# Kernel optimization log

Hardware: AMD Instinct MI355X
Metric: run time of the kernel (lower is better)

## Reference

```python
import jax, jax.numpy as jnp
import numpy as np

N = 20000        # nodes
E = 640000       # edges (before self-loops)
F_IN = 128
HID = 64
HEADS = 4
F_OUT = 128
G = 64           # graphs in batch
NEG_SLOPE = 0.2  # PyG GATConv leaky_relu default


def setup_inputs() -> dict:
    key = jax.random.key(0)
    ks = jax.random.split(key, 16)
    s = 0.05
    x = jax.random.normal(ks[0], (N, F_IN), jnp.float32)
    edge_index = jax.random.randint(ks[1], (2, E), 0, N, dtype=jnp.int64)
    batch = jnp.sort(jax.random.randint(ks[2], (N,), 0, G, dtype=jnp.int64))
    # layer 1: F_IN -> HID x HEADS (concat)
    W1 = jax.random.normal(ks[3], (F_IN, HEADS * HID), jnp.float32) * s
    a_src1 = jax.random.normal(ks[4], (HEADS, HID), jnp.float32) * s
    a_dst1 = jax.random.normal(ks[5], (HEADS, HID), jnp.float32) * s
    b1 = jnp.zeros((HEADS * HID,), jnp.float32)
    # layer 2: HEADS*HID -> HID x HEADS (concat)
    W2 = jax.random.normal(ks[6], (HEADS * HID, HEADS * HID), jnp.float32) * s
    a_src2 = jax.random.normal(ks[7], (HEADS, HID), jnp.float32) * s
    a_dst2 = jax.random.normal(ks[8], (HEADS, HID), jnp.float32) * s
    b2 = jnp.zeros((HEADS * HID,), jnp.float32)
    # layer 3: HEADS*HID -> F_OUT, heads=1, concat=False (mean)
    W3 = jax.random.normal(ks[9], (HEADS * HID, F_OUT), jnp.float32) * s
    a_src3 = jax.random.normal(ks[10], (1, F_OUT), jnp.float32) * s
    a_dst3 = jax.random.normal(ks[11], (1, F_OUT), jnp.float32) * s
    b3 = jnp.zeros((F_OUT,), jnp.float32)
    return dict(x=x, edge_index=edge_index, batch=batch,
                W1=W1, a_src1=a_src1, a_dst1=a_dst1, b1=b1,
                W2=W2, a_src2=a_src2, a_dst2=a_dst2, b2=b2,
                W3=W3, a_src3=a_src3, a_dst3=a_dst3, b3=b3)


def _gat_layer(x, src, dst, W, a_s, a_d, b, heads, concat):
    n = x.shape[0]
    h = (x @ W).reshape(n, heads, -1)                # [N,H,C]
    alpha_s = (h * a_s[None]).sum(-1)                # [N,H]
    alpha_d = (h * a_d[None]).sum(-1)                # [N,H]
    e = jax.nn.leaky_relu(alpha_s[src] + alpha_d[dst], NEG_SLOPE)  # [E,H]
    # segment softmax over incoming edges of each dst node
    m = jax.ops.segment_max(e, dst, num_segments=n)
    ex = jnp.exp(e - m[dst])
    denom = jax.ops.segment_sum(ex, dst, num_segments=n)
    alpha = ex / (denom[dst] + 1e-16)                # [E,H]
    out = jax.ops.segment_sum(alpha[:, :, None] * h[src], dst, num_segments=n)  # [N,H,C]
    out = out.reshape(n, -1) if concat else out.mean(axis=1)
    return out + b


def reference(x, edge_index, batch, W1, a_src1, a_dst1, b1,
              W2, a_src2, a_dst2, b2, W3, a_src3, a_dst3, b3):
    n = x.shape[0]
    # add self loops (PyG GATConv default add_self_loops=True)
    loop = jnp.arange(n, dtype=edge_index.dtype)
    src = jnp.concatenate([edge_index[0], loop])
    dst = jnp.concatenate([edge_index[1], loop])

    h = _gat_layer(x, src, dst, W1, a_src1, a_dst1, b1, HEADS, True)
    h = jax.nn.elu(h)
    h = _gat_layer(h, src, dst, W2, a_src2, a_dst2, b2, HEADS, True)
    h = jax.nn.elu(h)
    h = _gat_layer(h, src, dst, W3, a_src3, a_dst3, b3, 1, False)

    # global mean pool over graphs
    sums = jax.ops.segment_sum(h, batch, num_segments=G)
    cnts = jax.ops.segment_sum(jnp.ones((n, 1), h.dtype), batch, num_segments=G)
    graph_embedding = sums / jnp.maximum(cnts, 1.0)
    return graph_embedding, h
```

## Files before the change

### kernel.cpp

```cpp
#include <hip/hip_runtime.h>
#include <hip/hip_bf16.h>
#include <math.h>

#define N_NODES 20000
#define N_EDGES 640000
#define ET_EDGES (N_EDGES + N_NODES)
#define G_GRAPHS 64
#define NEG_SLOPE 0.2f


__global__ void hist_dst(const int* __restrict__ ei, int* __restrict__ cnt,
                         const int* __restrict__ batch, int* __restrict__ gstart) {
    int j = blockIdx.x * blockDim.x + threadIdx.x;
    if (blockIdx.x == 0 && threadIdx.x <= G_GRAPHS) {
        int g = threadIdx.x;
        int lo = 0, hi = N_NODES;
        while (lo < hi) {
            int mid = (lo + hi) >> 1;
            if (batch[mid] < g) lo = mid + 1; else hi = mid;
        }
        gstart[g] = lo;
    }
    if (j >= ET_EDGES) return;
    int d = (j < N_EDGES) ? ei[N_EDGES + j] : (j - N_EDGES);
    atomicAdd(&cnt[d], 1);
}

__global__ __launch_bounds__(1024) void scan_rowptr(const int* __restrict__ cnt,
                                                    int* __restrict__ row_ptr) {
    __shared__ int sums[1024];
    const int n = N_NODES;
    const int CH = (n + 1023) / 1024;
    int t = threadIdx.x;
    int base = t * CH;
    int s = 0;
    for (int i = 0; i < CH; ++i) {
        int idx = base + i;
        if (idx < n) s += cnt[idx];
    }
    sums[t] = s;
    __syncthreads();
    for (int o = 1; o < 1024; o <<= 1) {
        int v = (t >= o) ? sums[t - o] : 0;
        __syncthreads();
        sums[t] += v;
        __syncthreads();
    }
    int run = (t == 0) ? 0 : sums[t - 1];
    for (int i = 0; i < CH; ++i) {
        int idx = base + i;
        if (idx < n) { row_ptr[idx] = run; run += cnt[idx]; }
    }
    if (t == 1023) row_ptr[n] = sums[1023];
}

__global__ void fill_csr(const int* __restrict__ ei, const int* __restrict__ row_ptr,
                         int* __restrict__ cur, int* __restrict__ col) {
    int j = blockIdx.x * blockDim.x + threadIdx.x;
    if (j >= ET_EDGES) return;
    int s, d;
    if (j < N_EDGES) { s = ei[j]; d = ei[N_EDGES + j]; }
    else             { s = d = j - N_EDGES; }
    int pos = row_ptr[d] + atomicAdd(&cur[d], 1);
    col[pos] = s;
}


__global__ __launch_bounds__(256) void sgemm64(const float* __restrict__ A,
                                               const float* __restrict__ B,
                                               float* __restrict__ C,
                                               int M, int K, int Nc) {
    __shared__ float As[16][64];
    __shared__ float Bs[16][64];
    int bm = blockIdx.x * 64;
    int bn = blockIdx.y * 64;
    int t = threadIdx.x;
    int tr = t >> 2, tq = t & 3;
    int bkr = t >> 4, bnq = t & 15;
    int tm = (t >> 4) * 4;
    int tn = (t & 15) * 4;
    float acc[4][4] = {};
    for (int k0 = 0; k0 < K; k0 += 16) {
        int ar = bm + tr;
        float4 av = make_float4(0.f, 0.f, 0.f, 0.f);
        if (ar < M) av = *(const float4*)&A[(size_t)ar * K + k0 + tq * 4];
        As[tq * 4 + 0][tr] = av.x;
        As[tq * 4 + 1][tr] = av.y;
        As[tq * 4 + 2][tr] = av.z;
        As[tq * 4 + 3][tr] = av.w;
        float4 bv = *(const float4*)&B[(size_t)(k0 + bkr) * Nc + bn + bnq * 4];
        *(float4*)&Bs[bkr][bnq * 4] = bv;
        __syncthreads();
        #pragma unroll
        for (int k = 0; k < 16; ++k) {
            float a[4], b[4];
            *(float4*)a = *(const float4*)&As[k][tm];
            *(float4*)b = *(const float4*)&Bs[k][tn];
            #pragma unroll
            for (int i = 0; i < 4; ++i)
                #pragma unroll
                for (int j = 0; j < 4; ++j)
                    acc[i][j] = fmaf(a[i], b[j], acc[i][j]);
        }
        __syncthreads();
    }
    #pragma unroll
    for (int i = 0; i < 4; ++i) {
        int r = bm + tm + i;
        if (r < M) {
            float4 o = make_float4(acc[i][0], acc[i][1], acc[i][2], acc[i][3]);
            *(float4*)&C[(size_t)r * Nc + bn + tn] = o;
        }
    }
}


template <int HEADS, int C>
__global__ __launch_bounds__(256) void node_alpha2(const float* __restrict__ h,
                                                   const float* __restrict__ a_src,
                                                   const float* __restrict__ a_dst,
                                                   float* __restrict__ asT,
                                                   float* __restrict__ adT) {
    constexpr int F = HEADS * C;
    constexpr int VEC = F / 64;
    constexpr int LPH = C / VEC;
    int wid = threadIdx.x >> 6, lane = threadIdx.x & 63;
    int v = blockIdx.x * 4 + wid;
    if (v >= N_NODES) return;
    const float* hp = h + (size_t)v * F + lane * VEC;
    float ps = 0.f, pd = 0.f;
    #pragma unroll
    for (int c = 0; c < VEC; ++c) {
        float hv = hp[c];
        ps = fmaf(hv, a_src[lane * VEC + c], ps);
        pd = fmaf(hv, a_dst[lane * VEC + c], pd);
    }
    #pragma unroll
    for (int o = LPH / 2; o; o >>= 1) {
        ps += __shfl_xor(ps, o);
        pd += __shfl_xor(pd, o);
    }
    if ((lane & (LPH - 1)) == 0) {
        int head = lane / LPH;
        asT[head * N_NODES + v] = ps;
        adT[head * N_NODES + v] = pd;
    }
}


template <int NSLICE, int SCH, int F, int HEADS, bool DO_ELU>
__global__ __launch_bounds__(256) void gat_aggregate_sliced(
        const float* __restrict__ h,
        const float* __restrict__ asT,
        const float* __restrict__ adT,
        const int* __restrict__ row_ptr,
        const int* __restrict__ col,
        const float* __restrict__ bias,
        float* __restrict__ out) {
    constexpr int CL = SCH / 4;
    constexpr int E  = 64 / CL;
    constexpr int CPH = F / HEADS;
    __shared__ int   s_off[4][64];
    __shared__ float s_p[4][64];
    int slice = blockIdx.x & (NSLICE - 1);
    int ng = blockIdx.x >> 2;
    int wid = threadIdx.x >> 6, lane = threadIdx.x & 63;
    int v = ng * 4 + wid;
    if (v >= N_NODES) return;
    int head = (slice * SCH) / CPH;
    int eg = lane / CL, cl = lane % CL;
    int r0 = row_ptr[v], r1 = row_ptr[v + 1];
    float ad = adT[head * N_NODES + v];
    const float* asrc = asT + head * N_NODES;
    float acc[4] = {};
    float lsum = 0.f;
    const char* hb = (const char*)(h + slice * SCH + cl * 4);

#define GATHER4(gg)                                                        \
    {                                                                      \
        int k0 = ((gg) + 0) * E + eg;                                      \
        int k1 = ((gg) + 1) * E + eg;                                      \
        int k2 = ((gg) + 2) * E + eg;                                      \
        int k3 = ((gg) + 3) * E + eg;                                      \
        float p0 = s_p[wid][k0]; int o0 = s_off[wid][k0];                  \
        float p1 = s_p[wid][k1]; int o1 = s_off[wid][k1];                  \
        float p2 = s_p[wid][k2]; int o2 = s_off[wid][k2];                  \
        float p3 = s_p[wid][k3]; int o3 = s_off[wid][k3];                  \
        float4 h0 = *(const float4*)(hb + o0);                             \
        float4 h1 = *(const float4*)(hb + o1);                             \
        float4 h2 = *(const float4*)(hb + o2);                             \
        float4 h3 = *(const float4*)(hb + o3);                             \
        acc[0] = fmaf(p0, h0.x, acc[0]);                                   \
        acc[1] = fmaf(p0, h0.y, acc[1]);                                   \
        acc[2] = fmaf(p0, h0.z, acc[2]);                                   \
        acc[3] = fmaf(p0, h0.w, acc[3]);                                   \
        acc[0] = fmaf(p1, h1.x, acc[0]);                                   \
        acc[1] = fmaf(p1, h1.y, acc[1]);                                   \
        acc[2] = fmaf(p1, h1.z, acc[2]);                                   \
        acc[3] = fmaf(p1, h1.w, acc[3]);                                   \
        acc[0] = fmaf(p2, h2.x, acc[0]);                                   \
        acc[1] = fmaf(p2, h2.y, acc[1]);                                   \
        acc[2] = fmaf(p2, h2.z, acc[2]);                                   \
        acc[3] = fmaf(p2, h2.w, acc[3]);                                   \
        acc[0] = fmaf(p3, h3.x, acc[0]);                                   \
        acc[1] = fmaf(p3, h3.y, acc[1]);                                   \
        acc[2] = fmaf(p3, h3.z, acc[2]);                                   \
        acc[3] = fmaf(p3, h3.w, acc[3]);                                   \
    }

    for (int base = r0; base < r1; base += 64) {
        int j = base + lane;
        bool valid = j < r1;
        int s = col[valid ? j : r0];
        float e = asrc[s] + ad;
        e = (e > 0.f) ? e : NEG_SLOPE * e;
        float p = valid ? __expf(e) : 0.f;
        lsum += p;
        s_p[wid][lane] = p;
        s_off[wid][lane] = s * (F * 4);

        int nk = min(64, r1 - base);
        int nkg = (nk + E - 1) / E;
        int g = 0;
        for (; g + 4 <= nkg; g += 4) GATHER4(g);
        if (g < nkg) GATHER4(g);
    }
#undef GATHER4

    #pragma unroll
    for (int o = 32; o; o >>= 1) lsum += __shfl_xor(lsum, o);
    #pragma unroll
    for (int c = 0; c < 4; ++c) {
        #pragma unroll
        for (int o = CL; o < 64; o <<= 1) acc[c] += __shfl_xor(acc[c], o);
    }
    if (eg == 0) {
        float inv = 1.f / (lsum + 1e-16f);
        #pragma unroll
        for (int c = 0; c < 4; ++c) {
            int ch = slice * SCH + cl * 4 + c;
            float o = acc[c] * inv + bias[ch];
            if (DO_ELU) o = (o > 0.f) ? o : expm1f(o);
            out[(size_t)v * F + ch] = o;
        }
    }
}


__global__ void pool_mean4(const float* __restrict__ hout, const int* __restrict__ gstart,
                           float* __restrict__ gout) {
    int g = blockIdx.x;
    int q = blockIdx.y;
    int c = threadIdx.x;
    int off = gstart[g], end = gstart[g + 1];
    float inv = 1.f / fmaxf((float)(end - off), 1.0f);
    float s = 0.f;
    for (int i = off + q; i < end; i += 4) s += hout[(size_t)i * 128 + c];
    atomicAdd(&gout[g * 128 + c], s * inv);
}


static inline size_t align_up(size_t x, size_t a) { return (x + a - 1) & ~(a - 1); }

extern "C" void kernel_launch(void* const* d_in, const int* in_sizes, int n_in,
                              void* d_out, int out_size, void* d_ws, size_t ws_size,
                              hipStream_t stream) {
    const float* x   = (const float*)d_in[0];
    const int*   ei  = (const int*)d_in[1];
    const int*   bat = (const int*)d_in[2];
    const float* W1  = (const float*)d_in[3];
    const float* as1 = (const float*)d_in[4];
    const float* ad1 = (const float*)d_in[5];
    const float* b1  = (const float*)d_in[6];
    const float* W2  = (const float*)d_in[7];
    const float* as2 = (const float*)d_in[8];
    const float* ad2 = (const float*)d_in[9];
    const float* b2  = (const float*)d_in[10];
    const float* W3  = (const float*)d_in[11];
    const float* as3 = (const float*)d_in[12];
    const float* ad3 = (const float*)d_in[13];
    const float* b3  = (const float*)d_in[14];

    float* gout = (float*)d_out;
    float* hout = (float*)d_out + G_GRAPHS * 128;

    char* w = (char*)d_ws;
    size_t o = 0;
    float* bufA = (float*)(w + o); o = align_up(o + (size_t)N_NODES * 256 * 4, 256);
    float* bufB = (float*)(w + o); o = align_up(o + (size_t)N_NODES * 256 * 4, 256);
    float* asv  = (float*)(w + o); o = align_up(o + (size_t)N_NODES * 4 * 4, 256);
    float* adv  = (float*)(w + o); o = align_up(o + (size_t)N_NODES * 4 * 4, 256);
    int* row_ptr = (int*)(w + o);  o = align_up(o + (size_t)(N_NODES + 1) * 4, 256);
    int* col     = (int*)(w + o);  o = align_up(o + (size_t)ET_EDGES * 4, 256);
    int* cnt     = (int*)(w + o);  o += (size_t)N_NODES * 4;
    int* cur     = (int*)(w + o);  o = align_up(o + (size_t)N_NODES * 4, 256);
    int* gstart  = (int*)(w + o);  o = align_up(o + (size_t)(G_GRAPHS + 1) * 4, 256);

    hipMemsetAsync(cnt, 0, (size_t)N_NODES * 8, stream);
    hipMemsetAsync(gout, 0, (size_t)G_GRAPHS * 128 * 4, stream);
    hist_dst<<<(ET_EDGES + 255) / 256, 256, 0, stream>>>(ei, cnt, bat, gstart);
    scan_rowptr<<<1, 1024, 0, stream>>>(cnt, row_ptr);
    fill_csr<<<(ET_EDGES + 255) / 256, 256, 0, stream>>>(ei, row_ptr, cur, col);

    dim3 g4(313, 4), g2(313, 2);
    int nb = (N_NODES + 3) / 4;
    int nbs = nb * 4;

    sgemm64<<<g4, 256, 0, stream>>>(x, W1, bufA, N_NODES, 128, 256);
    node_alpha2<4, 64><<<nb, 256, 0, stream>>>(bufA, as1, ad1, asv, adv);
    gat_aggregate_sliced<4, 64, 256, 4, true><<<nbs, 256, 0, stream>>>(
        bufA, asv, adv, row_ptr, col, b1, bufB);

    sgemm64<<<g4, 256, 0, stream>>>(bufB, W2, bufA, N_NODES, 256, 256);
    node_alpha2<4, 64><<<nb, 256, 0, stream>>>(bufA, as2, ad2, asv, adv);
    gat_aggregate_sliced<4, 64, 256, 4, true><<<nbs, 256, 0, stream>>>(
        bufA, asv, adv, row_ptr, col, b2, bufB);

    sgemm64<<<g2, 256, 0, stream>>>(bufB, W3, bufA, N_NODES, 256, 128);
    node_alpha2<1, 128><<<nb, 256, 0, stream>>>(bufA, as3, ad3, asv, adv);
    gat_aggregate_sliced<4, 32, 128, 1, false><<<nbs, 256, 0, stream>>>(
        bufA, asv, adv, row_ptr, col, b3, hout);

    pool_mean4<<<dim3(G_GRAPHS, 4), 128, 0, stream>>>(hout, gstart, gout);
}
```

Baseline: 459.3 us.

## Replace fp32 SIMT GEMMs with split-bf16 MFMA GEMMs fed by aggregate epilogue

Swaps the scalar FMA sgemm for a matrix-core GEMM that represents each fp32 operand as a hi+lo bf16 pair and accumulates three bf16 MFMA products to keep near-fp32 accuracy. The aggregation epilogue of layers 1 and 2 now writes the activations directly as hi/lo bf16 arrays, and x and the weights are split (weights also transposed) in small pre-pass kernels. This targets the FP32 ALU cost of the three dense projections. In exchange it adds extra launches and split passes, and accuracy drops slightly from the dropped lo*lo term.

Measured after the change: 433.2 us. 1.06x faster.

```diff
diff --git a/kernel.cpp b/kernel.cpp
--- a/kernel.cpp
+++ b/kernel.cpp
@@ -7,6 +7,19 @@
 #define ET_EDGES (N_EDGES + N_NODES)
 #define G_GRAPHS 64
 #define NEG_SLOPE 0.2f
+
+typedef __attribute__((ext_vector_type(8))) short s8v;
+typedef __attribute__((ext_vector_type(4))) float f4v;
+
+__device__ __forceinline__ unsigned short bf_hi(float f) {
+    union { float f; unsigned int u; } c; c.f = f;
+    unsigned int r = (c.u + 0x7fffu + ((c.u >> 16) & 1u)) >> 16;
+    return (unsigned short)r;
+}
+__device__ __forceinline__ float bf_f(unsigned short h) {
+    union { unsigned int u; float f; } c; c.u = ((unsigned int)h) << 16;
+    return c.f;
+}
 
 
 __global__ void hist_dst(const int* __restrict__ ei, int* __restrict__ cnt,
@@ -66,52 +79,110 @@
 }
 
 
-__global__ __launch_bounds__(256) void sgemm64(const float* __restrict__ A,
-                                               const float* __restrict__ B,
-                                               float* __restrict__ C,
-                                               int M, int K, int Nc) {
-    __shared__ float As[16][64];
-    __shared__ float Bs[16][64];
-    int bm = blockIdx.x * 64;
-    int bn = blockIdx.y * 64;
-    int t = threadIdx.x;
-    int tr = t >> 2, tq = t & 3;
-    int bkr = t >> 4, bnq = t & 15;
-    int tm = (t >> 4) * 4;
-    int tn = (t & 15) * 4;
-    float acc[4][4] = {};
-    for (int k0 = 0; k0 < K; k0 += 16) {
-        int ar = bm + tr;
-        float4 av = make_float4(0.f, 0.f, 0.f, 0.f);
-        if (ar < M) av = *(const float4*)&A[(size_t)ar * K + k0 + tq * 4];
-        As[tq * 4 + 0][tr] = av.x;
-        As[tq * 4 + 1][tr] = av.y;
-        As[tq * 4 + 2][tr] = av.z;
-        As[tq * 4 + 3][tr] = av.w;
-        float4 bv = *(const float4*)&B[(size_t)(k0 + bkr) * Nc + bn + bnq * 4];
-        *(float4*)&Bs[bkr][bnq * 4] = bv;
+__global__ void split_f32(const float* __restrict__ in, unsigned short* __restrict__ hi,
+                          unsigned short* __restrict__ lo, int n) {
+    int i = (blockIdx.x * blockDim.x + threadIdx.x) * 4;
+    if (i >= n) return;
+    float4 v = *(const float4*)&in[i];
+    ushort4 h, l;
+    h.x = bf_hi(v.x); l.x = bf_hi(v.x - bf_f(h.x));
+    h.y = bf_hi(v.y); l.y = bf_hi(v.y - bf_f(h.y));
+    h.z = bf_hi(v.z); l.z = bf_hi(v.z - bf_f(h.z));
+    h.w = bf_hi(v.w); l.w = bf_hi(v.w - bf_f(h.w));
+    *(ushort4*)&hi[i] = h;
+    *(ushort4*)&lo[i] = l;
+}
+
+__global__ void wsplit(const float* __restrict__ W, unsigned short* __restrict__ th,
+                       unsigned short* __restrict__ tl, int K, int Nc) {
+    int idx = blockIdx.x * blockDim.x + threadIdx.x;
+    if (idx >= K * Nc) return;
+    int k = idx / Nc, n = idx % Nc;
+    float v = W[idx];
+    unsigned short h = bf_hi(v);
+    th[n * K + k] = h;
+    tl[n * K + k] = bf_hi(v - bf_f(h));
+}
+
+
+#define LDT 40
+
+__global__ __launch_bounds__(256) void gemm_split(
+        const unsigned short* __restrict__ Ah, const unsigned short* __restrict__ Al,
+        const unsigned short* __restrict__ Bh, const unsigned short* __restrict__ Bl,
+        float* __restrict__ C, int M, int Nc, int K) {
+    __shared__ unsigned short lAh[128 * LDT];
+    __shared__ unsigned short lAl[128 * LDT];
+    __shared__ unsigned short lBh[64 * LDT];
+    __shared__ unsigned short lBl[64 * LDT];
+    int bm = blockIdx.x * 128, bn = blockIdx.y * 64;
+    int t = threadIdx.x, w = t >> 6, lane = t & 63;
+    int wm = (w >> 1) * 64, wn = (w & 1) * 32;
+
+    f4v acc[4][2] = {};
+
+    int sr = t >> 1, sk = (t & 1) << 4;
+    int br = t >> 2, bk = (t & 3) << 3;
+    int ar = bm + sr; if (ar >= M) ar = M - 1;
+    const unsigned short* pAh = Ah + (size_t)ar * K + sk;
+    const unsigned short* pAl = Al + (size_t)ar * K + sk;
+    const unsigned short* pBh = Bh + (size_t)(bn + br) * K + bk;
+    const unsigned short* pBl = Bl + (size_t)(bn + br) * K + bk;
+
+    int fr = lane & 15, fk = (lane >> 4) << 3;
+
+    for (int k0 = 0; k0 < K; k0 += 32) {
+        uint4 vh0 = *(const uint4*)(pAh + k0);
+        uint4 vh1 = *(const uint4*)(pAh + k0 + 8);
+        uint4 vl0 = *(const uint4*)(pAl + k0);
+        uint4 vl1 = *(const uint4*)(pAl + k0 + 8);
+        uint4 wh  = *(const uint4*)(pBh + k0);
+        uint4 wl  = *(const uint4*)(pBl + k0);
         __syncthreads();
-        #pragma unroll
-        for (int k = 0; k < 16; ++k) {
-            float a[4], b[4];
-            *(float4*)a = *(const float4*)&As[k][tm];
-            *(float4*)b = *(const float4*)&Bs[k][tn];
+        *(uint4*)&lAh[sr * LDT + sk]     = vh0;
+        *(uint4*)&lAh[sr * LDT + sk + 8] = vh1;
+        *(uint4*)&lAl[sr * LDT + sk]     = vl0;
+        *(uint4*)&lAl[sr * LDT + sk + 8] = vl1;
+        *(uint4*)&lBh[br * LDT + bk] = wh;
+        *(uint4*)&lBl[br * LDT + bk] = wl;
+        __syncthreads();
+
+        s8v a_h[4], a_l[4], b_h[2], b_l[2];
+        #pragma unroll
+        for (int mi = 0; mi < 4; ++mi) {
+            a_h[mi] = *(const s8v*)&lAh[(wm + mi * 16 + fr) * LDT + fk];
+            a_l[mi] = *(const s8v*)&lAl[(wm + mi * 16 + fr) * LDT + fk];
+        }
+        #pragma unroll
+        for (int nj = 0; nj < 2; ++nj) {
+            b_h[nj] = *(const s8v*)&lBh[(wn + nj * 16 + fr) * LDT + fk];
+            b_l[nj] = *(const s8v*)&lBl[(wn + nj * 16 + fr) * LDT + fk];
+        }
+        #pragma unroll
+        for (int mi = 0; mi < 4; ++mi)
             #pragma unroll
-            for (int i = 0; i < 4; ++i)
-                #pragma unroll
-                for (int j = 0; j < 4; ++j)
-                    acc[i][j] = fmaf(a[i], b[j], acc[i][j]);
-        }
-        __syncthreads();
-    }
+            for (int nj = 0; nj < 2; ++nj) {
+                acc[mi][nj] = __builtin_amdgcn_mfma_f32_16x16x32_bf16(
+                    a_h[mi], b_h[nj], acc[mi][nj], 0, 0, 0);
+                acc[mi][nj] = __builtin_amdgcn_mfma_f32_16x16x32_bf16(
+                    a_h[mi], b_l[nj], acc[mi][nj], 0, 0, 0);
+                acc[mi][nj] = __builtin_amdgcn_mfma_f32_16x16x32_bf16(
+                    a_l[mi], b_h[nj], acc[mi][nj], 0, 0, 0);
+            }
+    }
+
     #pragma unroll
-    for (int i = 0; i < 4; ++i) {
-        int r = bm + tm + i;
-        if (r < M) {
-            float4 o = make_float4(acc[i][0], acc[i][1], acc[i][2], acc[i][3]);
-            *(float4*)&C[(size_t)r * Nc + bn + tn] = o;
-        }
-    }
+    for (int mi = 0; mi < 4; ++mi)
+        #pragma unroll
+        for (int nj = 0; nj < 2; ++nj) {
+            int row0 = bm + wm + mi * 16 + (lane >> 4) * 4;
+            int colc = bn + wn + nj * 16 + (lane & 15);
+            #pragma unroll
+            for (int q = 0; q < 4; ++q) {
+                int r = row0 + q;
+                if (r < M) C[(size_t)r * Nc + colc] = acc[mi][nj][q];
+            }
+        }
 }
 
 
@@ -148,7 +219,7 @@
 }
 
 
-template <int NSLICE, int SCH, int F, int HEADS, bool DO_ELU>
+template <int NSLICE, int SCH, int F, int HEADS, bool DO_ELU, bool SPLIT>
 __global__ __launch_bounds__(256) void gat_aggregate_sliced(
         const float* __restrict__ h,
         const float* __restrict__ asT,
@@ -156,7 +227,9 @@
         const int* __restrict__ row_ptr,
         const int* __restrict__ col,
         const float* __restrict__ bias,
-        float* __restrict__ out) {
+        float* __restrict__ out,
+        unsigned short* __restrict__ oh,
+        unsigned short* __restrict__ ol) {
     constexpr int CL = SCH / 4;
     constexpr int E  = 64 / CL;
     constexpr int CPH = F / HEADS;
@@ -236,12 +309,25 @@
     }
     if (eg == 0) {
         float inv = 1.f / (lsum + 1e-16f);
+        int ch0 = slice * SCH + cl * 4;
+        float o4[4];
         #pragma unroll
         for (int c = 0; c < 4; ++c) {
-            int ch = slice * SCH + cl * 4 + c;
-            float o = acc[c] * inv + bias[ch];
+            float o = acc[c] * inv + bias[ch0 + c];
             if (DO_ELU) o = (o > 0.f) ? o : expm1f(o);
-            out[(size_t)v * F + ch] = o;
+            o4[c] = o;
+        }
+        if (SPLIT) {
+            ushort4 hv, lv;
+            hv.x = bf_hi(o4[0]); lv.x = bf_hi(o4[0] - bf_f(hv.x));
+            hv.y = bf_hi(o4[1]); lv.y = bf_hi(o4[1] - bf_f(hv.y));
+            hv.z = bf_hi(o4[2]); lv.z = bf_hi(o4[2] - bf_f(hv.z));
+            hv.w = bf_hi(o4[3]); lv.w = bf_hi(o4[3] - bf_f(hv.w));
+            *(ushort4*)&oh[(size_t)v * F + ch0] = hv;
+            *(ushort4*)&ol[(size_t)v * F + ch0] = lv;
+        } else {
+            *(float4*)&out[(size_t)v * F + ch0] =
+                make_float4(o4[0], o4[1], o4[2], o4[3]);
         }
     }
 }
@@ -286,8 +372,17 @@
 
     char* w = (char*)d_ws;
     size_t o = 0;
-    float* bufA = (float*)(w + o); o = align_up(o + (size_t)N_NODES * 256 * 4, 256);
-    float* bufB = (float*)(w + o); o = align_up(o + (size_t)N_NODES * 256 * 4, 256);
+    float* bufA = (float*)(w + o);           o = align_up(o + (size_t)N_NODES * 256 * 4, 256);
+    unsigned short* Bh = (unsigned short*)(w + o); o = align_up(o + (size_t)N_NODES * 256 * 2, 256);
+    unsigned short* Bl = (unsigned short*)(w + o); o = align_up(o + (size_t)N_NODES * 256 * 2, 256);
+    unsigned short* xh = (unsigned short*)(w + o); o = align_up(o + (size_t)N_NODES * 128 * 2, 256);
+    unsigned short* xl = (unsigned short*)(w + o); o = align_up(o + (size_t)N_NODES * 128 * 2, 256);
+    unsigned short* Wt1h = (unsigned short*)(w + o); o = align_up(o + (size_t)256 * 128 * 2, 256);
+    unsigned short* Wt1l = (unsigned short*)(w + o); o = align_up(o + (size_t)256 * 128 * 2, 256);
+    unsigned short* Wt2h = (unsigned short*)(w + o); o = align_up(o + (size_t)256 * 256 * 2, 256);
+    unsigned short* Wt2l = (unsigned short*)(w + o); o = align_up(o + (size_t)256 * 256 * 2, 256);
+    unsigned short* Wt3h = (unsigned short*)(w + o); o = align_up(o + (size_t)128 * 256 * 2, 256);
+    unsigned short* Wt3l = (unsigned short*)(w + o); o = align_up(o + (size_t)128 * 256 * 2, 256);
     float* asv  = (float*)(w + o); o = align_up(o + (size_t)N_NODES * 4 * 4, 256);
     float* adv  = (float*)(w + o); o = align_up(o + (size_t)N_NODES * 4 * 4, 256);
     int* row_ptr = (int*)(w + o);  o = align_up(o + (size_t)(N_NODES + 1) * 4, 256);
@@ -301,25 +396,29 @@
     hist_dst<<<(ET_EDGES + 255) / 256, 256, 0, stream>>>(ei, cnt, bat, gstart);
     scan_rowptr<<<1, 1024, 0, stream>>>(cnt, row_ptr);
     fill_csr<<<(ET_EDGES + 255) / 256, 256, 0, stream>>>(ei, row_ptr, cur, col);
-
-    dim3 g4(313, 4), g2(313, 2);
+    split_f32<<<(N_NODES * 128 / 4 + 255) / 256, 256, 0, stream>>>(x, xh, xl, N_NODES * 128);
+    wsplit<<<(128 * 256 + 255) / 256, 256, 0, stream>>>(W1, Wt1h, Wt1l, 128, 256);
+    wsplit<<<(256 * 256 + 255) / 256, 256, 0, stream>>>(W2, Wt2h, Wt2l, 256, 256);
+    wsplit<<<(256 * 128 + 255) / 256, 256, 0, stream>>>(W3, Wt3h, Wt3l, 256, 128);
+
+    int gm = (N_NODES + 127) / 128;
     int nb = (N_NODES + 3) / 4;
     int nbs = nb * 4;
 
-    sgemm64<<<g4, 256, 0, stream>>>(x, W1, bufA, N_NODES, 128, 256);
+    gemm_split<<<dim3(gm, 4), 256, 0, stream>>>(xh, xl, Wt1h, Wt1l, bufA, N_NODES, 256, 128);
     node_alpha2<4, 64><<<nb, 256, 0, stream>>>(bufA, as1, ad1, asv, adv);
-    gat_aggregate_sliced<4, 64, 256, 4, true><<<nbs, 256, 0, stream>>>(
-        bufA, asv, adv, row_ptr, col, b1, bufB);
-
-    sgemm64<<<g4, 256, 0, stream>>>(bufB, W2, bufA, N_NODES, 256, 256);
+    gat_aggregate_sliced<4, 64, 256, 4, true, true><<<nbs, 256, 0, stream>>>(
+        bufA, asv, adv, row_ptr, col, b1, nullptr, Bh, Bl);
+
+    gemm_split<<<dim3(gm, 4), 256, 0, stream>>>(Bh, Bl, Wt2h, Wt2l, bufA, N_NODES, 256, 256);
     node_alpha2<4, 64><<<nb, 256, 0, stream>>>(bufA, as2, ad2, asv, adv);
-    gat_aggregate_sliced<4, 64, 256, 4, true><<<nbs, 256, 0, stream>>>(
-        bufA, asv, adv, row_ptr, col, b2, bufB);
-
-    sgemm64<<<g2, 256, 0, stream>>>(bufB, W3, bufA, N_NODES, 256, 128);
+    gat_aggregate_sliced<4, 64, 256, 4, true, true><<<nbs, 256, 0, stream>>>(
+        bufA, asv, adv, row_ptr, col, b2, nullptr, Bh, Bl);
+
+    gemm_split<<<dim3(gm, 2), 256, 0, stream>>>(Bh, Bl, Wt3h, Wt3l, bufA, N_NODES, 128, 256);
     node_alpha2<1, 128><<<nb, 256, 0, stream>>>(bufA, as3, ad3, asv, adv);
-    gat_aggregate_sliced<4, 32, 128, 1, false><<<nbs, 256, 0, stream>>>(
-        bufA, asv, adv, row_ptr, col, b3, hout);
+    gat_aggregate_sliced<4, 32, 128, 1, false, false><<<nbs, 256, 0, stream>>>(
+        bufA, asv, adv, row_ptr, col, b3, hout, nullptr, nullptr);
 
     pool_mean4<<<dim3(G_GRAPHS, 4), 128, 0, stream>>>(hout, gstart, gout);
 }
```
